# Performance work log

Measured on AMD Instinct MI355X. Metric: run time of the kernel, lower is better.

Reference implementation:

```python
import jax, jax.numpy as jnp
import numpy as np

DIM = 192
TDIM = 192
HEADS = 6
WS = (2, 7, 7)
SS = (1, 3, 3)
MLP_HID = 4 * DIM
RANK = DIM // 8
EPS = 1e-6


def _rel_pos_index(ws):
    wd, wh, ww = ws
    coords = np.stack(np.meshgrid(np.arange(wd), np.arange(wh), np.arange(ww), indexing='ij'))
    cf = coords.reshape(3, -1)
    rel = (cf[:, :, None] - cf[:, None, :]).transpose(1, 2, 0).astype(np.int64)
    rel[..., 0] += wd - 1
    rel[..., 1] += wh - 1
    rel[..., 2] += ww - 1
    rel[..., 0] *= (2 * wh - 1) * (2 * ww - 1)
    rel[..., 1] *= (2 * ww - 1)
    return rel.sum(-1)  # (N, N)


def _window_partition(x, ws):
    B, D, H, W, C = x.shape
    x = x.reshape(B, D // ws[0], ws[0], H // ws[1], ws[1], W // ws[2], ws[2], C)
    return x.transpose(0, 1, 3, 5, 2, 4, 6, 7).reshape(-1, ws[0] * ws[1] * ws[2], C)


def _window_reverse(w, ws, B, D, H, W):
    x = w.reshape(B, D // ws[0], H // ws[1], W // ws[2], ws[0], ws[1], ws[2], -1)
    return x.transpose(0, 1, 4, 2, 5, 3, 6, 7).reshape(B, D, H, W, -1)


def _ln(x):
    m = x.mean(-1, keepdims=True)
    v = ((x - m) ** 2).mean(-1, keepdims=True)
    return (x - m) * jax.lax.rsqrt(v + EPS)


def _compute_mask_np(Dp, Hp, Wp, ws, ss):
    img = np.zeros((1, Dp, Hp, Wp, 1), dtype=np.float32)
    cnt = 0
    for d in (slice(0, -ws[0]), slice(-ws[0], -ss[0]), slice(-ss[0], None)):
        for h in (slice(0, -ws[1]), slice(-ws[1], -ss[1]), slice(-ss[1], None)):
            for w in (slice(0, -ws[2]), slice(-ws[2], -ss[2]), slice(-ss[2], None)):
                img[:, d, h, w, :] = cnt
                cnt += 1
    x = img.reshape(1, Dp // ws[0], ws[0], Hp // ws[1], ws[1], Wp // ws[2], ws[2], 1)
    mw = x.transpose(0, 1, 3, 5, 2, 4, 6, 7).reshape(-1, ws[0] * ws[1] * ws[2])
    am = mw[:, None, :] - mw[:, :, None]
    return np.where(am != 0, np.float32(-100.0), np.float32(0.0))


def setup_inputs() -> dict:
    key = jax.random.key(0)
    ks = jax.random.split(key, 16)
    B, D, H, W, C = 1, 16, 64, 128, DIM
    Dp = D + (-D) % WS[0]
    Hp = H + (-H) % WS[1]
    Wp = W + (-W) % WS[2]
    s = 0.02
    bias_tab = (2 * WS[0] - 1) * (2 * WS[1] - 1) * (2 * WS[2] - 1)
    return {
        'x': jax.random.normal(ks[0], (B, D, H, W, C), jnp.float32),
        'mask_matrix': jnp.asarray(_compute_mask_np(Dp, Hp, Wp, WS, SS)),
        't': jax.random.normal(ks[1], (B, TDIM), jnp.float32),
        'w_qkv': jax.random.normal(ks[2], (C, 3 * C), jnp.float32) * s,
        'b_qkv': jnp.zeros((3 * C,), jnp.float32),
        'rel_bias': jax.random.normal(ks[3], (bias_tab, HEADS), jnp.float32) * s,
        'w_proj': jax.random.normal(ks[4], (C, C), jnp.float32) * s,
        'b_proj': jnp.zeros((C,), jnp.float32),
        'w1': jax.random.normal(ks[5], (C, MLP_HID), jnp.float32) * s,
        'b1': jnp.zeros((MLP_HID,), jnp.float32),
        'w2': jax.random.normal(ks[6], (MLP_HID, C), jnp.float32) * s,
        'b2': jnp.zeros((C,), jnp.float32),
        'wa1': jax.random.normal(ks[7], (TDIM, RANK), jnp.float32) * s,
        'wa2': jax.random.normal(ks[8], (RANK, 6 * C), jnp.float32) * s,
        'ba2': jax.random.normal(ks[9], (6 * C,), jnp.float32) * s,
    }


def reference(x, mask_matrix, t, w_qkv, b_qkv, rel_bias, w_proj, b_proj, w1, b1, w2, b2, wa1, wa2, ba2):
    B, D, H, W, C = x.shape
    hd = C // HEADS
    # AdaLN modulation params
    mod = (jax.nn.silu(t) @ wa1) @ wa2 + ba2  # (B, 6C)
    sh_msa, sc_msa, g_msa, sh_mlp, sc_mlp, g_mlp = jnp.split(mod, 6, axis=1)

    def modulate(y, sh, sc):
        return y * (1 + sc[:, None, None, None, :]) + sh[:, None, None, None, :]

    shortcut = x
    y = modulate(_ln(x), sh_msa, sc_msa)
    # pad to window multiples
    pad_d, pad_h, pad_w = (-D) % WS[0], (-H) % WS[1], (-W) % WS[2]
    y = jnp.pad(y, ((0, 0), (0, pad_d), (0, pad_h), (0, pad_w), (0, 0)))
    Dp, Hp, Wp = D + pad_d, H + pad_h, W + pad_w
    # cyclic shift
    y = jnp.roll(y, (-SS[0], -SS[1], -SS[2]), axis=(1, 2, 3))
    xw = _window_partition(y, WS)  # (B*nW, N, C)
    N = xw.shape[1]
    qkv = (xw @ w_qkv + b_qkv).reshape(-1, N, 3, HEADS, hd)
    q, k, v = qkv[:, :, 0], qkv[:, :, 1], qkv[:, :, 2]
    scale = hd ** -0.5
    attn = jnp.einsum('bnhd,bmhd->bhnm', q * scale, k)  # (B*nW, H, N, N)
    rpi = _rel_pos_index(WS)
    bias = rel_bias[rpi.reshape(-1)].reshape(N, N, HEADS).transpose(2, 0, 1)
    attn = attn + bias[None]
    nW = mask_matrix.shape[0]
    attn = attn.reshape(B, nW, HEADS, N, N) + mask_matrix[None, :, None]
    attn = jax.nn.softmax(attn, axis=-1).reshape(-1, HEADS, N, N)
    out = jnp.einsum('bhnm,bmhd->bnhd', attn, v).reshape(-1, N, C)
    out = out @ w_proj + b_proj
    y = _window_reverse(out, WS, B, Dp, Hp, Wp)
    y = jnp.roll(y, (SS[0], SS[1], SS[2]), axis=(1, 2, 3))
    y = y[:, :D, :H, :W, :]
    x1 = shortcut + g_msa[:, None, None, None, :] * y
    y2 = modulate(_ln(x1), sh_mlp, sc_mlp)
    h = jax.nn.gelu(y2 @ w1 + b1, approximate=False) @ w2 + b2
    return x1 + g_mlp[:, None, None, None, :] * h
```

## Files before the change

kernel.cpp:

```cpp
#include <hip/hip_runtime.h>
#include <hip/hip_bf16.h>

typedef __bf16 bf16x8 __attribute__((ext_vector_type(8)));
typedef float  f32x4  __attribute__((ext_vector_type(4)));
typedef unsigned int u32x4 __attribute__((ext_vector_type(4)));
typedef __attribute__((address_space(3))) unsigned int lds_u32;
typedef const __attribute__((address_space(1))) unsigned int glb_u32;

__device__ inline unsigned short f2bf(float f) {
    union { __hip_bfloat16 h; unsigned short u; } cv;
    cv.h = __float2bfloat16(f);
    return cv.u;
}
__device__ inline float bf2f(unsigned short u) {
    union { unsigned int i; float f; } c; c.i = ((unsigned int)u) << 16; return c.f;
}

__device__ inline bf16x8 load8(const unsigned short* p) {
    uint2 lo = *(const uint2*)(p);
    uint2 hi = *(const uint2*)(p + 16);
    u32x4 v; v[0] = lo.x; v[1] = lo.y; v[2] = hi.x; v[3] = hi.y;
    return __builtin_bit_cast(bf16x8, v);
}

__device__ inline bf16x8 load8s(const unsigned short* rowbase, int lg, int r3) {
    int b0 = ((((lg >> 1)    ) ^ r3) << 4) + ((lg & 1) << 3);
    int b1 = ((((lg >> 1) + 2) ^ r3) << 4) + ((lg & 1) << 3);
    uint2 lo = *(const uint2*)((const char*)rowbase + b0);
    uint2 hi = *(const uint2*)((const char*)rowbase + b1);
    u32x4 v; v[0] = lo.x; v[1] = lo.y; v[2] = hi.x; v[3] = hi.y;
    return __builtin_bit_cast(bf16x8, v);
}

__device__ inline f32x4 mfma16(bf16x8 a, bf16x8 b, f32x4 c) {
    return __builtin_amdgcn_mfma_f32_16x16x32_bf16(a, b, c, 0, 0, 0);
}

__device__ inline bool winmapT(int gg, int& T) {
    int win = gg / 98, n = gg % 98;
    int wdi = win / 190, rem = win % 190, whi = rem / 19, wwi = rem % 19;
    int td = n / 49, th = (n / 7) % 7, tw = n % 7;
    int sd = (wdi * 2 + td + 1) & 15;
    int sh = whi * 7 + th + 3; if (sh >= 70) sh -= 70;
    int sw = wwi * 7 + tw + 3; if (sw >= 133) sw -= 133;
    if (sh < 64 && sw < 128) { T = (sd * 64 + sh) * 128 + sw; return true; }
    return false;
}

__device__ inline int xcd_swz(int orig, int nwg) {
    int q = nwg >> 3, r = nwg & 7;
    int xcd = orig & 7, idx = orig >> 3;
    return (xcd < r ? xcd * (q + 1) : r * (q + 1) + (xcd - r) * q) + idx;
}

__global__ __launch_bounds__(256) void mod_k(const float* __restrict__ t,
    const float* __restrict__ wa1, const float* __restrict__ wa2,
    const float* __restrict__ ba2, float* __restrict__ mod)
{
    __shared__ float st[192];
    __shared__ float a[24];
    int tid = threadIdx.x;
    if (tid < 192) { float x = t[tid]; st[tid] = x / (1.f + __expf(-x)); }
    __syncthreads();
    if (tid < 24) {
        float s = 0.f;
        for (int c = 0; c < 192; ++c) s += st[c] * wa1[c * 24 + tid];
        a[tid] = s;
    }
    __syncthreads();
    for (int j = tid; j < 1152; j += 256) {
        float s = ba2[j];
        for (int r = 0; r < 24; ++r) s += a[r] * wa2[r * 1152 + j];
        mod[j] = s;
    }
}

__global__ __launch_bounds__(256) void prep_k(
    const float* __restrict__ wqkv, const float* __restrict__ wproj,
    const float* __restrict__ w1, const float* __restrict__ w2,
    const float* __restrict__ relb,
    unsigned short* __restrict__ wqkvT, unsigned short* __restrict__ wprojT,
    unsigned short* __restrict__ w1T, unsigned short* __restrict__ w2T,
    unsigned short* __restrict__ btabF)
{
    int i = blockIdx.x * 256 + threadIdx.x;
    if (i < 110592) { int n = i / 192, k = i % 192; wqkvT[i] = f2bf(wqkv[k * 576 + n]); return; }
    i -= 110592;
    if (i < 36864)  { int n = i / 192, k = i % 192; wprojT[i] = f2bf(wproj[k * 192 + n]); return; }
    i -= 36864;
    if (i < 147456) { int n = i / 192, k = i % 192; w1T[i] = f2bf(w1[k * 768 + n]); return; }
    i -= 147456;
    if (i < 147456) { int n = i / 768, k = i % 768; w2T[i] = f2bf(w2[k * 192 + n]); return; }
    i -= 147456;
    if (i < 688128) {
        int mt = i / 86016, r1 = i % 86016;
        int h  = r1 / 14336, r2 = r1 % 14336;
        int fq = r2 / 2048,  r3 = r2 % 2048;
        int l16 = r3 / 128,  r4 = r3 % 128;
        int lg  = r4 / 32,   r5 = r4 % 32;
        int fkey = r5 / 4,   e  = r5 % 4;
        int q = fq * 16 + l16, key = fkey * 16 + lg * 4 + e;
        float val;
        if (fkey == 7 || q >= 98 || key >= 98) {
            val = -1e30f;
        } else {
            int tdn = q / 49, thn = (q / 7) % 7, twn = q % 7;
            int tdm = key / 49, thm = (key / 7) % 7, twm = key % 7;
            int idx = (tdn - tdm + 1) * 169 + (thn - thm + 6) * 13 + (twn - twm + 6);
            float b = relb[idx * 6 + h];
            int bd = mt & 1, bh = (mt >> 1) & 1, bw = (mt >> 2) & 1;
            int idn = (bd ? (tdn == 0 ? 1 : 2) : 0) * 9 + (bh ? (thn < 4 ? 1 : 2) : 0) * 3 + (bw ? (twn < 4 ? 1 : 2) : 0);
            int idm = (bd ? (tdm == 0 ? 1 : 2) : 0) * 9 + (bh ? (thm < 4 ? 1 : 2) : 0) * 3 + (bw ? (twm < 4 ? 1 : 2) : 0);
            val = b + ((idn != idm) ? -100.f : 0.f);
        }
        btabF[i] = f2bf(val);
    }
}

__global__ __launch_bounds__(256) void lnwin_k(const float* __restrict__ x,
    const float* __restrict__ mod, unsigned short* __restrict__ ywin)
{
    int tok = blockIdx.x * 4 + (threadIdx.x >> 6);
    int lane = threadIdx.x & 63;
    int T;
    size_t ob = (size_t)tok * 192;
    if (winmapT(tok, T)) {
        const float* p = x + (size_t)T * 192;
        float x0 = p[lane], xa = p[64 + lane], xb = p[128 + lane];
        float s = x0 + xa + xb, q = x0 * x0 + xa * xa + xb * xb;
        for (int m = 32; m; m >>= 1) { s += __shfl_xor(s, m); q += __shfl_xor(q, m); }
        float mean = s * (1.f / 192.f);
        float var  = q * (1.f / 192.f) - mean * mean;
        float rstd = rsqrtf(var + 1e-6f);
        ywin[ob + lane]       = f2bf((x0 - mean) * rstd * (1.f + mod[192 + lane])       + mod[lane]);
        ywin[ob + 64 + lane]  = f2bf((xa - mean) * rstd * (1.f + mod[192 + 64 + lane])  + mod[64 + lane]);
        ywin[ob + 128 + lane] = f2bf((xb - mean) * rstd * (1.f + mod[192 + 128 + lane]) + mod[128 + lane]);
    } else {
        ywin[ob + lane] = 0; ywin[ob + 64 + lane] = 0; ywin[ob + 128 + lane] = 0;
    }
}

__global__ __launch_bounds__(256) void ln2_k(const float* __restrict__ x1,
    const float* __restrict__ mod, unsigned short* __restrict__ y2)
{
    int tok = blockIdx.x * 4 + (threadIdx.x >> 6);
    int lane = threadIdx.x & 63;
    const float* p = x1 + (size_t)tok * 192;
    float x0 = p[lane], xa = p[64 + lane], xb = p[128 + lane];
    float s = x0 + xa + xb, q = x0 * x0 + xa * xa + xb * xb;
    for (int m = 32; m; m >>= 1) { s += __shfl_xor(s, m); q += __shfl_xor(q, m); }
    float mean = s * (1.f / 192.f);
    float var  = q * (1.f / 192.f) - mean * mean;
    float rstd = rsqrtf(var + 1e-6f);
    size_t ob = (size_t)tok * 192;
    y2[ob + lane]       = f2bf((x0 - mean) * rstd * (1.f + mod[768 + lane])       + mod[576 + lane]);
    y2[ob + 64 + lane]  = f2bf((xa - mean) * rstd * (1.f + mod[768 + 64 + lane])  + mod[576 + 64 + lane]);
    y2[ob + 128 + lane] = f2bf((xb - mean) * rstd * (1.f + mod[768 + 128 + lane]) + mod[576 + 128 + lane]);
}

template<int FN, int EPI>
__global__ __launch_bounds__(256) void gemm_k(
    const unsigned short* __restrict__ A, const unsigned short* __restrict__ BT,
    const float* __restrict__ bias, unsigned short* __restrict__ outB, float* outF,
    const float* __restrict__ auxF, const float* __restrict__ mod,
    int M, int N, int K, int nx)
{
    constexpr int BN = FN * 32;
    __shared__ unsigned short As[128 * 32];
    __shared__ unsigned short Bs[BN * 32];
    const int t = threadIdx.x;
    const int wg = xcd_swz(blockIdx.x, gridDim.x);
    const int n0 = (wg % nx) * BN, m0 = (wg / nx) * 128;
    const int wid = t >> 6, lane = t & 63;
    const int lg = lane >> 4, l16 = lane & 15;
    const int wm = (wid >> 1) * 64, wn = (wid & 1) * (FN * 16);
    f32x4 acc[4][FN] = {};

    int arow[2], acs[2];
    #pragma unroll
    for (int j = 0; j < 2; ++j) {
        int p = t + j * 256;
        arow[j] = p >> 2;
        acs[j] = (p & 3) ^ (arow[j] & 3);
    }

    for (int kk = 0; kk < K; kk += 32) {
        #pragma unroll
        for (int j = 0; j < 2; ++j) {
            int gr = m0 + arow[j];
            const unsigned short* src = A + (size_t)(gr < M ? gr : 0) * K + kk + acs[j] * 8;
            __builtin_amdgcn_global_load_lds((glb_u32*)src,
                (lds_u32*)((char*)As + wid * 1024 + j * 4096), 16, 0, 0);
        }
        #pragma unroll
        for (int j = 0; j < BN / 64; ++j) {
            int gn = n0 + arow[j];
            const unsigned short* src = BT + (size_t)(gn < N ? gn : 0) * K + kk + acs[j] * 8;
            __builtin_amdgcn_global_load_lds((glb_u32*)src,
                (lds_u32*)((char*)Bs + wid * 1024 + j * 4096), 16, 0, 0);
        }
        __syncthreads();
        bf16x8 af[4], bv[FN];
        #pragma unroll
        for (int i = 0; i < 4; ++i) {
            int r = wm + i * 16 + l16;
            af[i] = load8s(As + r * 32, lg, r & 3);
        }
        #pragma unroll
        for (int j = 0; j < FN; ++j) {
            int r = wn + j * 16 + l16;
            bv[j] = load8s(Bs + r * 32, lg, r & 3);
        }
        #pragma unroll
        for (int i = 0; i < 4; ++i)
        #pragma unroll
        for (int j = 0; j < FN; ++j)
            acc[i][j] = mfma16(af[i], bv[j], acc[i][j]);
        __syncthreads();
    }

    #pragma unroll
    for (int i = 0; i < 4; ++i)
    #pragma unroll
    for (int j = 0; j < FN; ++j) {
        int gcol = n0 + wn + j * 16 + l16;
        if (gcol >= N) continue;
        float b = bias[gcol];
        #pragma unroll
        for (int e = 0; e < 4; ++e) {
            int grow = m0 + wm + i * 16 + lg * 4 + e;
            if (grow >= M) continue;
            float v = acc[i][j][e] + b;
            if (EPI == 0) {
                int which = gcol / 192, hh = (gcol / 32) % 6, c = gcol & 31;
                outB[((size_t)(hh * 3 + which) * 148960 + grow) * 32 + c] = f2bf(v);
            } else if (EPI == 1) {
                float gl = 0.5f * v * (1.f + erff(v * 0.70710678118654752f));
                outB[(size_t)grow * N + gcol] = f2bf(gl);
            } else if (EPI == 2) {
                int T;
                if (winmapT(grow, T)) {
                    size_t idx = (size_t)T * 192 + gcol;
                    outF[idx] = auxF[idx] + mod[384 + gcol] * v;
                }
            } else {
                size_t idx = (size_t)grow * 192 + gcol;
                outF[idx] = outF[idx] + mod[960 + gcol] * v;
            }
        }
    }
}

__global__ __launch_bounds__(256) void attn_k(
    const unsigned short* __restrict__ qkv, const unsigned short* __restrict__ btabF,
    unsigned short* __restrict__ out)
{
    __shared__ __align__(16) unsigned short Ks[2][112 * 46];
    __shared__ __align__(16) unsigned short VT[2][32 * 142];

    const int wg = xcd_swz(blockIdx.x, 4560);
    const int h = wg / 760, wp = wg % 760;
    const int win0 = wp * 2;
    const int t = threadIdx.x;
    const int wid = t >> 6, lg = (t >> 4) & 3, l16 = t & 15;

    const unsigned short* Qg = qkv + (size_t)(h * 3 + 0) * 148960 * 32;
    const unsigned short* Kg = qkv + (size_t)(h * 3 + 1) * 148960 * 32;
    const unsigned short* Vg = qkv + (size_t)(h * 3 + 2) * 148960 * 32;

    const int w2 = wid & 1, fq0 = wid >> 1;
    const int win = win0 + w2;
    const size_t rb = (size_t)win * 98;
    const int wdi = win / 190, remw = win % 190, whi = remw / 19, wwi = remw % 19;
    const int mt = (wdi == 7 ? 1 : 0) | (whi == 9 ? 2 : 0) | (wwi == 18 ? 4 : 0);
    const unsigned short* btW = btabF + (size_t)(mt * 6 + h) * 14336;

    bf16x8 qa[4];
    #pragma unroll
    for (int i = 0; i < 4; ++i) {
        int fq = fq0 + 2 * i;
        int fqc = (fq < 7) ? fq : 0;
        qa[i] = load8(Qg + (rb + fqc * 16 + l16) * 32 + 4 * lg);
    }

    #pragma unroll
    for (int v2 = 0; v2 < 2; ++v2) {
        const size_t rbs = (size_t)(win0 + v2) * 98;
        for (int i = t; i < 392; i += 256) {
            int r = i >> 2, cg = (i & 3) * 8;
            uint4 k = *(const uint4*)(Kg + (rbs + r) * 32 + cg);
            *(uint2*)(&Ks[v2][r * 46 + cg])     = make_uint2(k.x, k.y);
            *(uint2*)(&Ks[v2][r * 46 + cg + 4]) = make_uint2(k.z, k.w);
        }
        for (int i = t; i < 14 * 32; i += 256) {
            int r = 98 + (i >> 5), c = i & 31;
            Ks[v2][r * 46 + c] = 0;
        }
        for (int i = t; i < 512; i += 256) {
            if (i < 392) {
                uint4 v = *(const uint4*)(Vg + (rbs + (i >> 2)) * 32 + (i & 3) * 8);
                const unsigned short* vp = (const unsigned short*)&v;
                int m = i >> 2, c0 = (i & 3) * 8;
                #pragma unroll
                for (int j = 0; j < 8; ++j) VT[v2][(c0 + j) * 142 + m] = vp[j];
            }
        }
        for (int i = t; i < 32 * 30; i += 256) {
            int c = i / 30, m = 98 + i % 30;
            VT[v2][c * 142 + m] = 0;
        }
    }
    __syncthreads();

    __builtin_amdgcn_s_setprio(1);
    const float SCALE = 0.17677669529663687f;
    const unsigned short* KsW = &Ks[w2][0];
    const unsigned short* VTW = &VT[w2][0];

    #pragma unroll
    for (int i = 0; i < 4; ++i) {
        const int fq = fq0 + 2 * i;
        if (fq >= 7) break;

        const uint4* bp = (const uint4*)(btW + fq * 2048 + l16 * 128 + lg * 32);
        uint4 b0 = bp[0], b1 = bp[1], b2 = bp[2], b3 = bp[3];
        const unsigned bt32[16] = {b0.x, b0.y, b0.z, b0.w, b1.x, b1.y, b1.z, b1.w,
                                   b2.x, b2.y, b2.z, b2.w, b3.x, b3.y, b3.z, b3.w};

        f32x4 acc[7];
        #pragma unroll
        for (int fk = 0; fk < 7; ++fk) {
            bf16x8 kb = load8(KsW + (fk * 16 + l16) * 46 + 4 * lg);
            f32x4 z = {};
            acc[fk] = mfma16(kb, qa[i], z);
        }

        float mx = -1e30f;
        #pragma unroll
        for (int fk = 0; fk < 7; ++fk)
        #pragma unroll
        for (int e = 0; e < 4; ++e) {
            unsigned short bu = (unsigned short)(bt32[fk * 2 + (e >> 1)] >> ((e & 1) * 16));
            float s = fmaf(acc[fk][e], SCALE, bf2f(bu));
            acc[fk][e] = s;
            mx = fmaxf(mx, s);
        }
        mx = fmaxf(mx, __shfl_xor(mx, 16));
        mx = fmaxf(mx, __shfl_xor(mx, 32));
        float sum = 0.f;
        #pragma unroll
        for (int fk = 0; fk < 7; ++fk)
        #pragma unroll
        for (int e = 0; e < 4; ++e) {
            float p = __expf(acc[fk][e] - mx);
            acc[fk][e] = p;
            sum += p;
        }
        sum += __shfl_xor(sum, 16);
        sum += __shfl_xor(sum, 32);
        float rinv = 1.f / sum;

        bf16x8 sa[4];
        #pragma unroll
        for (int ks = 0; ks < 4; ++ks) {
            u32x4 w;
            w[0] = (unsigned)f2bf(acc[2 * ks][0]) | ((unsigned)f2bf(acc[2 * ks][1]) << 16);
            w[1] = (unsigned)f2bf(acc[2 * ks][2]) | ((unsigned)f2bf(acc[2 * ks][3]) << 16);
            if (ks < 3) {
                w[2] = (unsigned)f2bf(acc[2 * ks + 1][0]) | ((unsigned)f2bf(acc[2 * ks + 1][1]) << 16);
                w[3] = (unsigned)f2bf(acc[2 * ks + 1][2]) | ((unsigned)f2bf(acc[2 * ks + 1][3]) << 16);
            } else {
                w[2] = 0u; w[3] = 0u;
            }
            sa[ks] = __builtin_bit_cast(bf16x8, w);
        }
        float rv[4];
        #pragma unroll
        for (int e = 0; e < 4; ++e) rv[e] = __shfl(rinv, lg * 4 + e);

        #pragma unroll
        for (int fn = 0; fn < 2; ++fn) {
            f32x4 o = {};
            #pragma unroll
            for (int ks = 0; ks < 4; ++ks) {
                bf16x8 vb = load8(VTW + (fn * 16 + l16) * 142 + ks * 32 + 4 * lg);
                o = mfma16(sa[ks], vb, o);
            }
            #pragma unroll
            for (int e = 0; e < 4; ++e) {
                int r = fq * 16 + lg * 4 + e;
                if (r < 98) {
                    out[(rb + r) * 192 + h * 32 + fn * 16 + l16] = f2bf(o[e] * rv[e]);
                }
            }
        }
    }
    __builtin_amdgcn_s_setprio(0);
}

extern "C" void kernel_launch(void* const* d_in, const int* in_sizes, int n_in,
                              void* d_out, int out_size, void* d_ws, size_t ws_size,
                              hipStream_t stream)
{
    const float* x      = (const float*)d_in[0];
    const float* tvec   = (const float*)d_in[2];
    const float* w_qkv  = (const float*)d_in[3];
    const float* b_qkv  = (const float*)d_in[4];
    const float* relb   = (const float*)d_in[5];
    const float* w_proj = (const float*)d_in[6];
    const float* b_proj = (const float*)d_in[7];
    const float* w1     = (const float*)d_in[8];
    const float* b1     = (const float*)d_in[9];
    const float* w2     = (const float*)d_in[10];
    const float* b2     = (const float*)d_in[11];
    const float* wa1    = (const float*)d_in[12];
    const float* wa2    = (const float*)d_in[13];
    const float* ba2    = (const float*)d_in[14];

    char* ws = (char*)d_ws;
    float*          mod    = (float*)ws;
    unsigned short* wqkvT  = (unsigned short*)(ws + 2101760);
    unsigned short* wprojT = (unsigned short*)(ws + 2322944);
    unsigned short* w1T    = (unsigned short*)(ws + 2396672);
    unsigned short* w2T    = (unsigned short*)(ws + 2691584);
    unsigned short* btabF  = (unsigned short*)(ws + 2986496);
    unsigned short* qkvb   = (unsigned short*)(ws + 4834304);
    unsigned short* h      = (unsigned short*)(ws + 4834304);
    unsigned short* attn_c = (unsigned short*)(ws + 176436224);
    unsigned short* ywin   = (unsigned short*)(ws + 233636864);
    unsigned short* y2b    = (unsigned short*)(ws + 290837504);
    float*          dout   = (float*)d_out;

    mod_k<<<1, 256, 0, stream>>>(tvec, wa1, wa2, ba2, mod);
    prep_k<<<4416, 256, 0, stream>>>(w_qkv, w_proj, w1, w2, relb, wqkvT, wprojT, w1T, w2T, btabF);
    lnwin_k<<<37240, 256, 0, stream>>>(x, mod, ywin);

    gemm_k<4, 0><<<5 * 1164, 256, 0, stream>>>(
        ywin, wqkvT, b_qkv, qkvb, nullptr, nullptr, mod, 148960, 576, 192, 5);
    attn_k<<<4560, 256, 0, stream>>>(qkvb, btabF, attn_c);
    gemm_k<2, 2><<<3 * 1164, 256, 0, stream>>>(
        attn_c, wprojT, b_proj, nullptr, dout, x, mod, 148960, 192, 192, 3);

    ln2_k<<<32768, 256, 0, stream>>>(dout, mod, y2b);

    gemm_k<4, 1><<<6 * 1024, 256, 0, stream>>>(
        y2b, w1T, b1, h, nullptr, nullptr, mod, 131072, 768, 192, 6);
    gemm_k<2, 3><<<3 * 1024, 256, 0, stream>>>(
        h, w2T, b2, nullptr, dout, nullptr, mod, 131072, 192, 768, 3);
}
```

Baseline: 957.1 us.

## Double-buffer LDS tiles in GEMM to overlap global loads with MFMA

Splits the shared A and B tiles into two buffers and issues the next K-slice's global-to-LDS loads before computing on the current slice. Row base pointers are hoisted out of the K loop. This is meant to hide global load latency behind the MFMA work, at the cost of doubling LDS use per block, which may reduce occupancy.

```diff
diff --git a/kernel.cpp b/kernel.cpp
--- a/kernel.cpp
+++ b/kernel.cpp
@@ -166,8 +166,8 @@
     int M, int N, int K, int nx)
 {
     constexpr int BN = FN * 32;
-    __shared__ unsigned short As[128 * 32];
-    __shared__ unsigned short Bs[BN * 32];
+    __shared__ unsigned short As[2][128 * 32];
+    __shared__ unsigned short Bs[2][BN * 32];
     const int t = threadIdx.x;
     const int wg = xcd_swz(blockIdx.x, gridDim.x);
     const int n0 = (wg % nx) * BN, m0 = (wg / nx) * 128;
@@ -183,33 +183,54 @@
         arow[j] = p >> 2;
         acs[j] = (p & 3) ^ (arow[j] & 3);
     }
-
-    for (int kk = 0; kk < K; kk += 32) {
-        #pragma unroll
-        for (int j = 0; j < 2; ++j) {
-            int gr = m0 + arow[j];
-            const unsigned short* src = A + (size_t)(gr < M ? gr : 0) * K + kk + acs[j] * 8;
-            __builtin_amdgcn_global_load_lds((glb_u32*)src,
-                (lds_u32*)((char*)As + wid * 1024 + j * 4096), 16, 0, 0);
-        }
-        #pragma unroll
-        for (int j = 0; j < BN / 64; ++j) {
-            int gn = n0 + arow[j];
-            const unsigned short* src = BT + (size_t)(gn < N ? gn : 0) * K + kk + acs[j] * 8;
-            __builtin_amdgcn_global_load_lds((glb_u32*)src,
-                (lds_u32*)((char*)Bs + wid * 1024 + j * 4096), 16, 0, 0);
-        }
-        __syncthreads();
+    const unsigned short* asrc[2];
+    const unsigned short* bsrc[BN / 64];
+    #pragma unroll
+    for (int j = 0; j < 2; ++j) {
+        int gr = m0 + arow[j];
+        asrc[j] = A + (size_t)(gr < M ? gr : 0) * K + acs[j] * 8;
+    }
+    #pragma unroll
+    for (int j = 0; j < BN / 64; ++j) {
+        int gn = n0 + arow[j];
+        bsrc[j] = BT + (size_t)(gn < N ? gn : 0) * K + acs[j] * 8;
+    }
+
+    const int NS = K >> 5;
+
+    #pragma unroll
+    for (int j = 0; j < 2; ++j)
+        __builtin_amdgcn_global_load_lds((glb_u32*)(asrc[j]),
+            (lds_u32*)((char*)&As[0][0] + wid * 1024 + j * 4096), 16, 0, 0);
+    #pragma unroll
+    for (int j = 0; j < BN / 64; ++j)
+        __builtin_amdgcn_global_load_lds((glb_u32*)(bsrc[j]),
+            (lds_u32*)((char*)&Bs[0][0] + wid * 1024 + j * 4096), 16, 0, 0);
+    __syncthreads();
+
+    for (int s = 0; s < NS; ++s) {
+        const int cur = s & 1;
+        if (s + 1 < NS) {
+            const int kk = (s + 1) << 5;
+            #pragma unroll
+            for (int j = 0; j < 2; ++j)
+                __builtin_amdgcn_global_load_lds((glb_u32*)(asrc[j] + kk),
+                    (lds_u32*)((char*)&As[cur ^ 1][0] + wid * 1024 + j * 4096), 16, 0, 0);
+            #pragma unroll
+            for (int j = 0; j < BN / 64; ++j)
+                __builtin_amdgcn_global_load_lds((glb_u32*)(bsrc[j] + kk),
+                    (lds_u32*)((char*)&Bs[cur ^ 1][0] + wid * 1024 + j * 4096), 16, 0, 0);
+        }
         bf16x8 af[4], bv[FN];
         #pragma unroll
         for (int i = 0; i < 4; ++i) {
             int r = wm + i * 16 + l16;
-            af[i] = load8s(As + r * 32, lg, r & 3);
+            af[i] = load8s(&As[cur][r * 32], lg, r & 3);
         }
         #pragma unroll
         for (int j = 0; j < FN; ++j) {
             int r = wn + j * 16 + l16;
-            bv[j] = load8s(Bs + r * 32, lg, r & 3);
+            bv[j] = load8s(&Bs[cur][r * 32], lg, r & 3);
         }
         #pragma unroll
         for (int i = 0; i < 4; ++i)
```

Result: faster. 928.8 us (-3.0%).
